# Optimization experiments

Measured on AMD Instinct MI355X. Metric: run time of the kernel, lower is better.

The kernel has to match this reference:

```python
import jax, jax.numpy as jnp
import numpy as np

DOWNSAMPLE = 4
REG = 0.05
SINKHORN_ITERS = 50
LAMBDA_OT = 1.0
LAMBDA_TV = 1.0


def setup_inputs() -> dict:
    key = jax.random.key(0)
    k1, k2 = jax.random.split(key)
    pred = jax.random.uniform(k1, (16, 1, 256, 256), dtype=jnp.float32)
    gt = jax.random.uniform(k2, (16, 1, 256, 256), dtype=jnp.float32)
    return {"pred": pred, "gt": gt, "epoch": 5, "max_epoch": 10}


def _avg_pool(x, k):
    B, C, H, W = x.shape
    return x.reshape(B, C, H // k, k, W // k, k).mean(axis=(3, 5))


def _normalize(x, n):
    # relu then normalize to a distribution; fall back to uniform if sum==0
    x = jnp.maximum(x, 0.0)
    s = x.sum(axis=1, keepdims=True)  # [B,1]
    return jnp.where(s > 0, x / s, jnp.full_like(x, 1.0 / n))


def _curriculum_loss(pred, gt, epoch, max_epoch):
    B = pred.shape[0]
    # --- counting loss: L1 between total counts ---
    pc = pred.reshape(B, -1).sum(axis=1)
    gc = gt.reshape(B, -1).sum(axis=1)
    l_count = jnp.abs(pc - gc).mean()

    t = float(epoch) / float(max(1, max_epoch))
    ot_w = LAMBDA_OT * t
    tv_w = LAMBDA_TV * t

    # --- OT loss (batched Sinkhorn) ---
    pd = _avg_pool(pred, DOWNSAMPLE)
    gd = _avg_pool(gt, DOWNSAMPLE)
    h, w = pd.shape[2], pd.shape[3]
    n = h * w
    ys = jnp.arange(h, dtype=jnp.float32)
    xs = jnp.arange(w, dtype=jnp.float32)
    yy, xx = jnp.meshgrid(ys, xs, indexing="ij")
    yf = yy.reshape(-1)  # [n]
    xf = xx.reshape(-1)
    # squared euclidean cost matrix [n,n], built separably (no [n,n,2] temp)
    M = (yf[:, None] - yf[None, :]) ** 2 + (xf[:, None] - xf[None, :]) ** 2
    K = jnp.exp(-M / REG)  # [n,n]

    a = _normalize(pd.reshape(B, -1), n)  # [B,n]
    b = _normalize(gd.reshape(B, -1), n)

    def step(uv, _):
        u, v = uv
        u = a / (v @ K.T)  # K @ v per sample, batched
        v = b / (u @ K)    # K.T @ u per sample, batched
        return (u, v), None

    ones = jnp.ones((B, n), dtype=pred.dtype)
    (u, v), _ = jax.lax.scan(step, (ones, ones), None, length=SINKHORN_ITERS)
    # cost_b = sum_ij u_i K_ij v_j M_ij
    cost = jnp.einsum("bn,nm,bm->b", u, K * M, v)
    l_ot = cost.mean()

    # --- total variation loss ---
    dx = jnp.abs(pred[:, :, :, 1:] - pred[:, :, :, :-1]).mean()
    dy = jnp.abs(pred[:, :, 1:, :] - pred[:, :, :-1, :]).mean()
    l_tv = dx + dy

    return l_count + ot_w * l_ot + tv_w * l_tv


def reference(pred, gt, epoch, max_epoch):
    return _curriculum_loss(pred, gt, epoch, max_epoch)
```

## Files before the change

### kernel.cpp

```cpp
#include <hip/hip_runtime.h>
#include <math.h>


#define KW1 2.0611536224385578e-09f
#define MW2 8.4967085105831778e-18f
#define SP 68
#define RP 72

__device__ __forceinline__ float ad4(const float4 a, const float4 b) {
  return fabsf(a.x - b.x) + fabsf(a.y - b.y) + fabsf(a.z - b.z) + fabsf(a.w - b.w);
}

__device__ __forceinline__ void hrow(const float f[4], int tx, float h[4]) {
  float l = __shfl_up(f[3], 1, 16);
  float r = __shfl_down(f[0], 1, 16);
  l = (tx == 0) ? 0.f : l;
  r = (tx == 15) ? 0.f : r;
  h[0] = fmaf(KW1, l + f[1], f[0]);
  h[1] = fmaf(KW1, f[0] + f[2], f[1]);
  h[2] = fmaf(KW1, f[1] + f[3], f[2]);
  h[3] = fmaf(KW1, f[2] + r, f[3]);
}

__device__ __forceinline__ void half_step(
    const float prev[4][4], const float h0[4], const float h3[4],
    const float cf[4][4],
    const float* __restrict__ HB_rd, const float* __restrict__ HT_rd,
    float* __restrict__ HT_wr, float* __restrict__ HB_wr,
    int hbr, int htr, int htw, int tx,
    float out[4][4], float oh0[4], float oh3[4]) {
  const float4 hm4 = *(const float4*)&HB_rd[hbr];
  const float4 hp4 = *(const float4*)&HT_rd[htr];
  float h1[4], h2[4];
  hrow(prev[1], tx, h1);
  hrow(prev[2], tx, h2);
  const float m[4] = {hm4.x, hm4.y, hm4.z, hm4.w};
  const float p[4] = {hp4.x, hp4.y, hp4.z, hp4.w};
#pragma unroll
  for (int j = 0; j < 4; ++j) {
    out[0][j] = cf[0][j] * __builtin_amdgcn_rcpf(fmaf(KW1, m[j] + h1[j], h0[j]));
    out[1][j] = cf[1][j] * __builtin_amdgcn_rcpf(fmaf(KW1, h0[j] + h2[j], h1[j]));
    out[2][j] = cf[2][j] * __builtin_amdgcn_rcpf(fmaf(KW1, h1[j] + h3[j], h2[j]));
    out[3][j] = cf[3][j] * __builtin_amdgcn_rcpf(fmaf(KW1, h2[j] + p[j], h3[j]));
  }
  hrow(out[0], tx, oh0);
  hrow(out[3], tx, oh3);
  *(float4*)&HT_wr[htw] = make_float4(oh0[0], oh0[1], oh0[2], oh0[3]);
  *(float4*)&HB_wr[htw] = make_float4(oh3[0], oh3[1], oh3[2], oh3[3]);
}

__global__ __launch_bounds__(256) void fused_kernel(
    const float* __restrict__ pred, const float* __restrict__ gt,
    float* __restrict__ ws, const int* __restrict__ epoch,
    const int* __restrict__ max_epoch, float* __restrict__ out,
    unsigned int* __restrict__ cnt) {
  __shared__ float HTu[18 * SP], HBu[18 * SP], HTv[18 * SP], HBv[18 * SP];
  __shared__ float RTs[18 * RP], RBs[18 * RP];
  __shared__ float rbuf[24];

  const int b = blockIdx.x;
  const int t = threadIdx.x;
  const int tyg = t >> 4, tx = t & 15;
  const int y0 = tyg * 4, x0 = tx * 4;

  for (int i = t; i < 18 * SP; i += 256) {
    HTu[i] = 0.f; HBu[i] = 0.f; HTv[i] = 0.f; HBv[i] = 0.f;
  }
  for (int i = t; i < 18 * RP; i += 256) { RTs[i] = 0.f; RBs[i] = 0.f; }

  const float* pb = pred + b * 65536;
  const float* gb = gt + b * 65536;
  const int sr0 = 4 * y0, sc0 = 4 * x0;

  float pd[4][4], gd[4][4];
  float4 pr0, pr1, pr2, pr3;
  float spraw = 0.f, sgraw = 0.f, sx = 0.f, sy = 0.f;
#pragma unroll
  for (int i = 0; i < 4; ++i) {
    float a0 = 0.f, a1 = 0.f, a2 = 0.f, a3 = 0.f;
    float c0 = 0.f, c1 = 0.f, c2 = 0.f, c3 = 0.f;
#pragma unroll 1
    for (int rr = 0; rr < 4; ++rr) {
      const int r = i * 4 + rr;
      const float* prow = pb + (sr0 + r) * 256 + sc0;
      const float4 q0 = *(const float4*)(prow);
      const float4 q1 = *(const float4*)(prow + 4);
      const float4 q2 = *(const float4*)(prow + 8);
      const float4 q3 = *(const float4*)(prow + 12);
      const float s0 = (q0.x + q0.y) + (q0.z + q0.w);
      const float s1 = (q1.x + q1.y) + (q1.z + q1.w);
      const float s2 = (q2.x + q2.y) + (q2.z + q2.w);
      const float s3 = (q3.x + q3.y) + (q3.z + q3.w);
      a0 += s0; a1 += s1; a2 += s2; a3 += s3;
      spraw += (s0 + s1) + (s2 + s3);
      sx += fabsf(q0.y - q0.x) + fabsf(q0.z - q0.y) + fabsf(q0.w - q0.z)
          + fabsf(q1.x - q0.w)
          + fabsf(q1.y - q1.x) + fabsf(q1.z - q1.y) + fabsf(q1.w - q1.z)
          + fabsf(q2.x - q1.w)
          + fabsf(q2.y - q2.x) + fabsf(q2.z - q2.y) + fabsf(q2.w - q2.z)
          + fabsf(q3.x - q2.w)
          + fabsf(q3.y - q3.x) + fabsf(q3.z - q3.y) + fabsf(q3.w - q3.z);
      const float nf = __shfl_down(q0.x, 1, 16);
      if (tx < 15) sx += fabsf(nf - q3.w);
      if (r > 0) sy += ad4(q0, pr0) + ad4(q1, pr1) + ad4(q2, pr2) + ad4(q3, pr3);
      pr0 = q0; pr1 = q1; pr2 = q2; pr3 = q3;
      const float* grow = gb + (sr0 + r) * 256 + sc0;
      const float4 g0 = *(const float4*)(grow);
      const float4 g1 = *(const float4*)(grow + 4);
      const float4 g2 = *(const float4*)(grow + 8);
      const float4 g3 = *(const float4*)(grow + 12);
      const float u0 = (g0.x + g0.y) + (g0.z + g0.w);
      const float u1 = (g1.x + g1.y) + (g1.z + g1.w);
      const float u2 = (g2.x + g2.y) + (g2.z + g2.w);
      const float u3 = (g3.x + g3.y) + (g3.z + g3.w);
      c0 += u0; c1 += u1; c2 += u2; c3 += u3;
      sgraw += (u0 + u1) + (u2 + u3);
    }
    pd[i][0] = a0; pd[i][1] = a1; pd[i][2] = a2; pd[i][3] = a3;
    gd[i][0] = c0; gd[i][1] = c1; gd[i][2] = c2; gd[i][3] = c3;
  }
  if (tyg < 15) {
    const float* prow = pb + (sr0 + 16) * 256 + sc0;
    sy += ad4(*(const float4*)(prow), pr0) + ad4(*(const float4*)(prow + 4), pr1)
        + ad4(*(const float4*)(prow + 8), pr2) + ad4(*(const float4*)(prow + 12), pr3);
  }

  float spd = 0.f, sgd = 0.f;
#pragma unroll
  for (int i = 0; i < 4; ++i)
#pragma unroll
    for (int j = 0; j < 4; ++j) {
      pd[i][j] = fmaxf(pd[i][j] * 0.0625f, 0.f); spd += pd[i][j];
      gd[i][j] = fmaxf(gd[i][j] * 0.0625f, 0.f); sgd += gd[i][j];
    }

  float r0 = spraw, r1 = sgraw, r2 = spd, r3 = sgd, r4 = sx, r5 = sy;
#pragma unroll
  for (int o = 32; o > 0; o >>= 1) {
    r0 += __shfl_down(r0, o); r1 += __shfl_down(r1, o);
    r2 += __shfl_down(r2, o); r3 += __shfl_down(r3, o);
    r4 += __shfl_down(r4, o); r5 += __shfl_down(r5, o);
  }
  if ((t & 63) == 0) {
    const int w = t >> 6;
    rbuf[w * 6 + 0] = r0; rbuf[w * 6 + 1] = r1; rbuf[w * 6 + 2] = r2;
    rbuf[w * 6 + 3] = r3; rbuf[w * 6 + 4] = r4; rbuf[w * 6 + 5] = r5;
  }
  __syncthreads();
  if (t == 0) {
    float a0 = 0, a1 = 0, a2 = 0, a3 = 0, a4 = 0, a5 = 0;
    for (int w = 0; w < 4; ++w) {
      a0 += rbuf[w * 6 + 0]; a1 += rbuf[w * 6 + 1]; a2 += rbuf[w * 6 + 2];
      a3 += rbuf[w * 6 + 3]; a4 += rbuf[w * 6 + 4]; a5 += rbuf[w * 6 + 5];
    }
    ws[b] = a0; ws[16 + b] = a1; ws[48 + b] = a4; ws[64 + b] = a5;
    rbuf[0] = a2; rbuf[1] = a3;
  }
  __syncthreads();
  const float Sp = rbuf[0], Sg = rbuf[1];

  float av[4][4], bv[4][4];
#pragma unroll
  for (int i = 0; i < 4; ++i)
#pragma unroll
    for (int j = 0; j < 4; ++j) {
      av[i][j] = (Sp > 0.f) ? (pd[i][j] / Sp) : (1.f / 4096.f);
      bv[i][j] = (Sg > 0.f) ? (gd[i][j] / Sg) : (1.f / 4096.f);
    }

  const int htw = (1 + tyg) * SP + x0;
  const int hbr = tyg * SP + x0;
  const int htr = (2 + tyg) * SP + x0;

  float uu[4][4], vv[4][4], hu0[4], hu3[4], hv0[4], hv3[4];
#pragma unroll
  for (int i = 0; i < 4; ++i)
#pragma unroll
    for (int j = 0; j < 4; ++j) vv[i][j] = 1.f;
  hrow(vv[0], tx, hv0);
  hrow(vv[3], tx, hv3);
  *(float4*)&HTv[htw] = make_float4(hv0[0], hv0[1], hv0[2], hv0[3]);
  *(float4*)&HBv[htw] = make_float4(hv3[0], hv3[1], hv3[2], hv3[3]);
  __syncthreads();

#pragma unroll 1
  for (int it = 0; it < 50; ++it) {
    half_step(vv, hv0, hv3, av, HBv, HTv, HTu, HBu, hbr, htr, htw, tx,
              uu, hu0, hu3);
    __syncthreads();
    half_step(uu, hu0, hu3, bv, HBu, HTu, HTv, HBv, hbr, htr, htw, tx,
              vv, hv0, hv3);
    __syncthreads();
  }

  *(float2*)&RTs[(1 + tyg) * RP + 2 + x0] = make_float2(vv[0][0], vv[0][1]);
  *(float2*)&RTs[(1 + tyg) * RP + 4 + x0] = make_float2(vv[0][2], vv[0][3]);
  *(float2*)&RBs[(1 + tyg) * RP + 2 + x0] = make_float2(vv[3][0], vv[3][1]);
  *(float2*)&RBs[(1 + tyg) * RP + 4 + x0] = make_float2(vv[3][2], vv[3][3]);
  __syncthreads();
  float c = 0.f;
  {
    const float4 t0 = *(const float4*)&RBs[tyg * RP + x0];
    const float4 t1 = *(const float4*)&RBs[tyg * RP + x0 + 4];
    const float4 b0 = *(const float4*)&RTs[(tyg + 2) * RP + x0];
    const float4 b1 = *(const float4*)&RTs[(tyg + 2) * RP + x0 + 4];
    float W[6][6];
    W[0][0] = t0.y; W[0][1] = t0.z; W[0][2] = t0.w;
    W[0][3] = t1.x; W[0][4] = t1.y; W[0][5] = t1.z;
    W[5][0] = b0.y; W[5][1] = b0.z; W[5][2] = b0.w;
    W[5][3] = b1.x; W[5][4] = b1.y; W[5][5] = b1.z;
#pragma unroll
    for (int i = 0; i < 4; ++i) {
      float l = __shfl_up(vv[i][3], 1, 16);
      float r = __shfl_down(vv[i][0], 1, 16);
      W[1 + i][0] = (tx == 0) ? 0.f : l;
      W[1 + i][5] = (tx == 15) ? 0.f : r;
#pragma unroll
      for (int j = 0; j < 4; ++j) W[1 + i][1 + j] = vv[i][j];
    }
#pragma unroll
    for (int i = 0; i < 4; ++i)
#pragma unroll
      for (int j = 0; j < 4; ++j) {
        const float e = (W[i][j + 1] + W[i + 2][j + 1])
                      + (W[i + 1][j] + W[i + 1][j + 2]);
        const float d = (W[i][j] + W[i][j + 2])
                      + (W[i + 2][j] + W[i + 2][j + 2]);
        c += uu[i][j] * fmaf(MW2, d, KW1 * e);
      }
  }
#pragma unroll
  for (int o = 32; o > 0; o >>= 1) c += __shfl_down(c, o);
  if ((t & 63) == 0) rbuf[t >> 6] = c;
  __syncthreads();
  if (t == 0) {
    ws[32 + b] = rbuf[0] + rbuf[1] + rbuf[2] + rbuf[3];
    __threadfence();
    const unsigned int old = atomicAdd(cnt, 1u);
    if (old == 15u) {
      __threadfence();
      float lc = 0.f, lot = 0.f, tvx = 0.f, tvy = 0.f;
      for (int k = 0; k < 16; ++k) {
        const float p  = __hip_atomic_load(&ws[k],      __ATOMIC_RELAXED, __HIP_MEMORY_SCOPE_AGENT);
        const float g  = __hip_atomic_load(&ws[16 + k], __ATOMIC_RELAXED, __HIP_MEMORY_SCOPE_AGENT);
        const float ct = __hip_atomic_load(&ws[32 + k], __ATOMIC_RELAXED, __HIP_MEMORY_SCOPE_AGENT);
        const float x  = __hip_atomic_load(&ws[48 + k], __ATOMIC_RELAXED, __HIP_MEMORY_SCOPE_AGENT);
        const float y  = __hip_atomic_load(&ws[64 + k], __ATOMIC_RELAXED, __HIP_MEMORY_SCOPE_AGENT);
        lc += fabsf(p - g); lot += ct; tvx += x; tvy += y;
      }
      int me = max_epoch[0]; if (me < 1) me = 1;
      const float tt = (float)epoch[0] / (float)me;
      const float ltv = tvx / (16.f * 256.f * 255.f) + tvy / (16.f * 255.f * 256.f);
      out[0] = lc * (1.f / 16.f) + tt * (lot * (1.f / 16.f)) + tt * ltv;
    }
  }
}

extern "C" void kernel_launch(void* const* d_in, const int* in_sizes, int n_in,
                              void* d_out, int out_size, void* d_ws, size_t ws_size,
                              hipStream_t stream) {
  const float* pred = (const float*)d_in[0];
  const float* gt   = (const float*)d_in[1];
  const int* epoch  = (const int*)d_in[2];
  const int* max_ep = (const int*)d_in[3];
  float* out = (float*)d_out;
  float* ws  = (float*)d_ws;
  unsigned int* cnt = (unsigned int*)((char*)d_ws + 384);

  hipMemsetAsync(cnt, 0, 4, stream);
  fused_kernel<<<dim3(16), dim3(256), 0, stream>>>(pred, gt, ws, epoch,
                                                   max_ep, out, cnt);
}
```

Baseline: 123.5 us.

## Use DPP row shifts and compute interior Sinkhorn rows off the barrier path

Replaces ds_bpermute-based shuffles with DPP row_shr/row_shl moves (bound_ctrl zero fill at row edges), so neighbour exchange within 16-lane rows is cheaper. Shared memory now holds raw boundary rows, with halo columns, instead of horizontally pre-filtered rows. Each thread recomputes the horizontal filter of its neighbours' rows locally. The interior rows 1-2 of each half-step are deferred and computed after the barrier alongside the next phase, which shortens the critical path between barriers. This trades some extra arithmetic and wider LDS reads for fewer shuffles and less work between synchronisations.

```diff
diff --git a/kernel.cpp b/kernel.cpp
--- a/kernel.cpp
+++ b/kernel.cpp
@@ -4,49 +4,55 @@
 
 #define KW1 2.0611536224385578e-09f
 #define MW2 8.4967085105831778e-18f
-#define SP 68
-#define RP 72
+#define RP2 72
+
+__device__ __forceinline__ float dpp_left(float x) {
+  return __int_as_float(__builtin_amdgcn_update_dpp(
+      0, __float_as_int(x), 0x111, 0xF, 0xF, true));
+}
+__device__ __forceinline__ float dpp_right(float x) {
+  return __int_as_float(__builtin_amdgcn_update_dpp(
+      0, __float_as_int(x), 0x101, 0xF, 0xF, true));
+}
 
 __device__ __forceinline__ float ad4(const float4 a, const float4 b) {
   return fabsf(a.x - b.x) + fabsf(a.y - b.y) + fabsf(a.z - b.z) + fabsf(a.w - b.w);
 }
 
-__device__ __forceinline__ void hrow(const float f[4], int tx, float h[4]) {
-  float l = __shfl_up(f[3], 1, 16);
-  float r = __shfl_down(f[0], 1, 16);
-  l = (tx == 0) ? 0.f : l;
-  r = (tx == 15) ? 0.f : r;
+__device__ __forceinline__ void hrow4(const float f[4], float h[4]) {
+  const float l = dpp_left(f[3]);
+  const float r = dpp_right(f[0]);
   h[0] = fmaf(KW1, l + f[1], f[0]);
   h[1] = fmaf(KW1, f[0] + f[2], f[1]);
   h[2] = fmaf(KW1, f[1] + f[3], f[2]);
   h[3] = fmaf(KW1, f[2] + r, f[3]);
 }
 
-__device__ __forceinline__ void half_step(
-    const float prev[4][4], const float h0[4], const float h3[4],
-    const float cf[4][4],
-    const float* __restrict__ HB_rd, const float* __restrict__ HT_rd,
-    float* __restrict__ HT_wr, float* __restrict__ HB_wr,
-    int hbr, int htr, int htw, int tx,
-    float out[4][4], float oh0[4], float oh3[4]) {
-  const float4 hm4 = *(const float4*)&HB_rd[hbr];
-  const float4 hp4 = *(const float4*)&HT_rd[htr];
-  float h1[4], h2[4];
-  hrow(prev[1], tx, h1);
-  hrow(prev[2], tx, h2);
-  const float m[4] = {hm4.x, hm4.y, hm4.z, hm4.w};
-  const float p[4] = {hp4.x, hp4.y, hp4.z, hp4.w};
-#pragma unroll
-  for (int j = 0; j < 4; ++j) {
-    out[0][j] = cf[0][j] * __builtin_amdgcn_rcpf(fmaf(KW1, m[j] + h1[j], h0[j]));
-    out[1][j] = cf[1][j] * __builtin_amdgcn_rcpf(fmaf(KW1, h0[j] + h2[j], h1[j]));
-    out[2][j] = cf[2][j] * __builtin_amdgcn_rcpf(fmaf(KW1, h1[j] + h3[j], h2[j]));
-    out[3][j] = cf[3][j] * __builtin_amdgcn_rcpf(fmaf(KW1, h2[j] + p[j], h3[j]));
-  }
-  hrow(out[0], tx, oh0);
-  hrow(out[3], tx, oh3);
-  *(float4*)&HT_wr[htw] = make_float4(oh0[0], oh0[1], oh0[2], oh0[3]);
-  *(float4*)&HB_wr[htw] = make_float4(oh3[0], oh3[1], oh3[2], oh3[3]);
+__device__ __forceinline__ void phase_core(
+    const float prev[4][4], float ph[4][4],
+    const float cf0[4], const float cf3[4],
+    float2 mA, float4 mB, float2 mC, float2 pA, float4 pB, float2 pC,
+    float* __restrict__ RT_wr, float* __restrict__ RB_wr, int wb,
+    float out0[4], float out3[4]) {
+  hrow4(prev[0], ph[0]); hrow4(prev[1], ph[1]);
+  hrow4(prev[2], ph[2]); hrow4(prev[3], ph[3]);
+  float hm[4], hp[4];
+  hm[0] = fmaf(KW1, mA.y + mB.y, mB.x);
+  hm[1] = fmaf(KW1, mB.x + mB.z, mB.y);
+  hm[2] = fmaf(KW1, mB.y + mB.w, mB.z);
+  hm[3] = fmaf(KW1, mB.z + mC.x, mB.w);
+  hp[0] = fmaf(KW1, pA.y + pB.y, pB.x);
+  hp[1] = fmaf(KW1, pB.x + pB.z, pB.y);
+  hp[2] = fmaf(KW1, pB.y + pB.w, pB.z);
+  hp[3] = fmaf(KW1, pB.z + pC.x, pB.w);
+#pragma unroll
+  for (int j = 0; j < 4; ++j)
+    out0[j] = cf0[j] * __builtin_amdgcn_rcpf(fmaf(KW1, hm[j] + ph[1][j], ph[0][j]));
+#pragma unroll
+  for (int j = 0; j < 4; ++j)
+    out3[j] = cf3[j] * __builtin_amdgcn_rcpf(fmaf(KW1, ph[2][j] + hp[j], ph[3][j]));
+  *(float4*)&RT_wr[wb] = make_float4(out0[0], out0[1], out0[2], out0[3]);
+  *(float4*)&RB_wr[wb] = make_float4(out3[0], out3[1], out3[2], out3[3]);
 }
 
 __global__ __launch_bounds__(256) void fused_kernel(
@@ -54,8 +60,8 @@
     float* __restrict__ ws, const int* __restrict__ epoch,
     const int* __restrict__ max_epoch, float* __restrict__ out,
     unsigned int* __restrict__ cnt) {
-  __shared__ float HTu[18 * SP], HBu[18 * SP], HTv[18 * SP], HBv[18 * SP];
-  __shared__ float RTs[18 * RP], RBs[18 * RP];
+  __shared__ float RTu[18 * RP2], RBu[18 * RP2];
+  __shared__ float RTv[18 * RP2], RBv[18 * RP2];
   __shared__ float rbuf[24];
 
   const int b = blockIdx.x;
@@ -63,10 +69,9 @@
   const int tyg = t >> 4, tx = t & 15;
   const int y0 = tyg * 4, x0 = tx * 4;
 
-  for (int i = t; i < 18 * SP; i += 256) {
-    HTu[i] = 0.f; HBu[i] = 0.f; HTv[i] = 0.f; HBv[i] = 0.f;
-  }
-  for (int i = t; i < 18 * RP; i += 256) { RTs[i] = 0.f; RBs[i] = 0.f; }
+  for (int i = t; i < 18 * RP2; i += 256) {
+    RTu[i] = 0.f; RBu[i] = 0.f; RTv[i] = 0.f; RBv[i] = 0.f;
+  }
 
   const float* pb = pred + b * 65536;
   const float* gb = gt + b * 65536;
@@ -100,7 +105,7 @@
           + fabsf(q2.y - q2.x) + fabsf(q2.z - q2.y) + fabsf(q2.w - q2.z)
           + fabsf(q3.x - q2.w)
           + fabsf(q3.y - q3.x) + fabsf(q3.z - q3.y) + fabsf(q3.w - q3.z);
-      const float nf = __shfl_down(q0.x, 1, 16);
+      const float nf = dpp_right(q0.x);
       if (tx < 15) sx += fabsf(nf - q3.w);
       if (r > 0) sy += ad4(q0, pr0) + ad4(q1, pr1) + ad4(q2, pr2) + ad4(q3, pr3);
       pr0 = q0; pr1 = q1; pr2 = q2; pr3 = q3;
@@ -168,53 +173,80 @@
       bv[i][j] = (Sg > 0.f) ? (gd[i][j] / Sg) : (1.f / 4096.f);
     }
 
-  const int htw = (1 + tyg) * SP + x0;
-  const int hbr = tyg * SP + x0;
-  const int htr = (2 + tyg) * SP + x0;
-
-  float uu[4][4], vv[4][4], hu0[4], hu3[4], hv0[4], hv3[4];
+  const int rbb = tyg * RP2 + x0 + 2;
+  const int rtb = (tyg + 2) * RP2 + x0 + 2;
+  const int wb  = (1 + tyg) * RP2 + 4 + x0;
+
+  float uu[4][4], vv[4][4], uh[4][4], vh[4][4];
 #pragma unroll
   for (int i = 0; i < 4; ++i)
 #pragma unroll
     for (int j = 0; j < 4; ++j) vv[i][j] = 1.f;
-  hrow(vv[0], tx, hv0);
-  hrow(vv[3], tx, hv3);
-  *(float4*)&HTv[htw] = make_float4(hv0[0], hv0[1], hv0[2], hv0[3]);
-  *(float4*)&HBv[htw] = make_float4(hv3[0], hv3[1], hv3[2], hv3[3]);
+  *(float4*)&RTv[wb] = make_float4(1.f, 1.f, 1.f, 1.f);
+  *(float4*)&RBv[wb] = make_float4(1.f, 1.f, 1.f, 1.f);
   __syncthreads();
 
 #pragma unroll 1
   for (int it = 0; it < 50; ++it) {
-    half_step(vv, hv0, hv3, av, HBv, HTv, HTu, HBu, hbr, htr, htw, tx,
-              uu, hu0, hu3);
+    {
+      const float2 mA = *(const float2*)&RBv[rbb];
+      const float4 mB = *(const float4*)&RBv[rbb + 2];
+      const float2 mC = *(const float2*)&RBv[rbb + 6];
+      const float2 pA = *(const float2*)&RTv[rtb];
+      const float4 pB = *(const float4*)&RTv[rtb + 2];
+      const float2 pC = *(const float2*)&RTv[rtb + 6];
+      if (it != 0) {
+#pragma unroll
+        for (int j = 0; j < 4; ++j) {
+          vv[1][j] = bv[1][j] * __builtin_amdgcn_rcpf(fmaf(KW1, uh[0][j] + uh[2][j], uh[1][j]));
+          vv[2][j] = bv[2][j] * __builtin_amdgcn_rcpf(fmaf(KW1, uh[1][j] + uh[3][j], uh[2][j]));
+        }
+      }
+      phase_core(vv, vh, av[0], av[3], mA, mB, mC, pA, pB, pC,
+                 RTu, RBu, wb, uu[0], uu[3]);
+    }
     __syncthreads();
-    half_step(uu, hu0, hu3, bv, HBu, HTu, HTv, HBv, hbr, htr, htw, tx,
-              vv, hv0, hv3);
+    {
+      const float2 mA = *(const float2*)&RBu[rbb];
+      const float4 mB = *(const float4*)&RBu[rbb + 2];
+      const float2 mC = *(const float2*)&RBu[rbb + 6];
+      const float2 pA = *(const float2*)&RTu[rtb];
+      const float4 pB = *(const float4*)&RTu[rtb + 2];
+      const float2 pC = *(const float2*)&RTu[rtb + 6];
+#pragma unroll
+      for (int j = 0; j < 4; ++j) {
+        uu[1][j] = av[1][j] * __builtin_amdgcn_rcpf(fmaf(KW1, vh[0][j] + vh[2][j], vh[1][j]));
+        uu[2][j] = av[2][j] * __builtin_amdgcn_rcpf(fmaf(KW1, vh[1][j] + vh[3][j], vh[2][j]));
+      }
+      phase_core(uu, uh, bv[0], bv[3], mA, mB, mC, pA, pB, pC,
+                 RTv, RBv, wb, vv[0], vv[3]);
+    }
     __syncthreads();
   }
 
-  *(float2*)&RTs[(1 + tyg) * RP + 2 + x0] = make_float2(vv[0][0], vv[0][1]);
-  *(float2*)&RTs[(1 + tyg) * RP + 4 + x0] = make_float2(vv[0][2], vv[0][3]);
-  *(float2*)&RBs[(1 + tyg) * RP + 2 + x0] = make_float2(vv[3][0], vv[3][1]);
-  *(float2*)&RBs[(1 + tyg) * RP + 4 + x0] = make_float2(vv[3][2], vv[3][3]);
-  __syncthreads();
+#pragma unroll
+  for (int j = 0; j < 4; ++j) {
+    vv[1][j] = bv[1][j] * __builtin_amdgcn_rcpf(fmaf(KW1, uh[0][j] + uh[2][j], uh[1][j]));
+    vv[2][j] = bv[2][j] * __builtin_amdgcn_rcpf(fmaf(KW1, uh[1][j] + uh[3][j], uh[2][j]));
+  }
+
   float c = 0.f;
   {
-    const float4 t0 = *(const float4*)&RBs[tyg * RP + x0];
-    const float4 t1 = *(const float4*)&RBs[tyg * RP + x0 + 4];
-    const float4 b0 = *(const float4*)&RTs[(tyg + 2) * RP + x0];
-    const float4 b1 = *(const float4*)&RTs[(tyg + 2) * RP + x0 + 4];
+    const float2 mA = *(const float2*)&RBv[rbb];
+    const float4 mB = *(const float4*)&RBv[rbb + 2];
+    const float2 mC = *(const float2*)&RBv[rbb + 6];
+    const float2 pA = *(const float2*)&RTv[rtb];
+    const float4 pB = *(const float4*)&RTv[rtb + 2];
+    const float2 pC = *(const float2*)&RTv[rtb + 6];
     float W[6][6];
-    W[0][0] = t0.y; W[0][1] = t0.z; W[0][2] = t0.w;
-    W[0][3] = t1.x; W[0][4] = t1.y; W[0][5] = t1.z;
-    W[5][0] = b0.y; W[5][1] = b0.z; W[5][2] = b0.w;
-    W[5][3] = b1.x; W[5][4] = b1.y; W[5][5] = b1.z;
+    W[0][0] = mA.y; W[0][1] = mB.x; W[0][2] = mB.y;
+    W[0][3] = mB.z; W[0][4] = mB.w; W[0][5] = mC.x;
+    W[5][0] = pA.y; W[5][1] = pB.x; W[5][2] = pB.y;
+    W[5][3] = pB.z; W[5][4] = pB.w; W[5][5] = pC.x;
 #pragma unroll
     for (int i = 0; i < 4; ++i) {
-      float l = __shfl_up(vv[i][3], 1, 16);
-      float r = __shfl_down(vv[i][0], 1, 16);
-      W[1 + i][0] = (tx == 0) ? 0.f : l;
-      W[1 + i][5] = (tx == 15) ? 0.f : r;
+      W[1 + i][0] = dpp_left(vv[i][3]);
+      W[1 + i][5] = dpp_right(vv[i][0]);
 #pragma unroll
       for (int j = 0; j < 4; ++j) W[1 + i][1 + j] = vv[i][j];
     }
```

After: 120.8 us. 2.2% less time.
